# Kernel tuning notes

Hardware: AMD Instinct MI355X
Metric: run time of the kernel (lower is better)

The kernel has to match this reference:

```python
import jax, jax.numpy as jnp
import numpy as np

WH, WW = 7, 7
N = WH * WW
DIM = 384
HEADS = 12
NW = 64          # windows per image
B_ = 2048        # batch * NW


def _relative_position_index():
    ch, cw = np.meshgrid(np.arange(WH), np.arange(WW), indexing='ij')
    coords = np.stack([ch, cw]).reshape(2, -1)                      # [2, N]
    rel = coords[:, :, None] - coords[:, None, :]                   # [2, N, N]
    rel = rel.transpose(1, 2, 0)
    rel[:, :, 0] += WH - 1
    rel[:, :, 1] += WW - 1
    rel[:, :, 0] *= 2 * WW - 1
    return jnp.asarray(rel.sum(-1), dtype=jnp.int32)                # [N, N]


def setup_inputs() -> dict:
    key = jax.random.key(0)
    ks = jax.random.split(key, 7)
    return {
        'x': jax.random.normal(ks[0], (B_, N, DIM), dtype=jnp.float32),
        'qkv_w': jax.random.normal(ks[1], (3 * DIM, DIM), dtype=jnp.float32) * 0.02,
        'qkv_b': jax.random.normal(ks[2], (3 * DIM,), dtype=jnp.float32) * 0.02,
        'proj_w': jax.random.normal(ks[3], (DIM, DIM), dtype=jnp.float32) * 0.02,
        'proj_b': jax.random.normal(ks[4], (DIM,), dtype=jnp.float32) * 0.02,
        'bias_table': jax.random.normal(ks[5], ((2 * WH - 1) * (2 * WW - 1), HEADS), dtype=jnp.float32) * 0.02,
        'mask': jax.random.normal(ks[6], (NW, N, N), dtype=jnp.float32),
        'rel_idx': _relative_position_index(),
    }


def reference(x, qkv_w, qkv_b, proj_w, proj_b, bias_table, mask, rel_idx):
    B_, n, C = x.shape
    H = HEADS
    hd = C // H
    scale = hd ** (-0.5)

    qkv = x @ qkv_w.T + qkv_b                                        # [B_, N, 3C]
    qkv = qkv.reshape(B_, n, 3, H, hd).transpose(2, 0, 3, 1, 4)      # [3, B_, H, N, hd]
    q, k, v = qkv[0], qkv[1], qkv[2]

    attn = jnp.einsum('bhqd,bhkd->bhqk', q * scale, k)               # [B_, H, N, N]

    rpb = bias_table[rel_idx.reshape(-1)].reshape(n, n, H)           # gather [N, N, H]
    attn = attn + rpb.transpose(2, 0, 1)[None]                       # [B_, H, N, N]

    nW = mask.shape[0]
    attn = attn.reshape(B_ // nW, nW, H, n, n) + mask[None, :, None]
    attn = attn.reshape(B_, H, n, n)
    attn = jax.nn.softmax(attn, axis=-1)

    out = jnp.einsum('bhqk,bhkd->bhqd', attn, v)                     # [B_, H, N, hd]
    out = out.transpose(0, 2, 1, 3).reshape(B_, n, C)
    return out @ proj_w.T + proj_b
```

## Files before the change

kernel.cpp:

```cpp
#include <hip/hip_runtime.h>
#include <hip/hip_bf16.h>
#include <cstdint>
#include <cstddef>

#define NTOK 49
#define DIM 384
#define KDIM 384
#define HEADS 12
#define HD 32
#define BATCH 2048
#define MROWS (BATCH * NTOK)

typedef unsigned short u16;
typedef __bf16 bf16x8 __attribute__((ext_vector_type(8)));
typedef unsigned short u16x8 __attribute__((ext_vector_type(8)));
typedef float f32x4 __attribute__((ext_vector_type(4)));

__device__ __forceinline__ u16 f2b(float f) {
  union { float f; unsigned u; } v; v.f = f;
  unsigned r = v.u + 0x7fffu + ((v.u >> 16) & 1u);
  return (u16)(r >> 16);
}

__device__ __forceinline__ bf16x8 ld_bf8(const u16* p) {
  u16x8 u = *(const u16x8*)p;
  return __builtin_bit_cast(bf16x8, u);
}

__device__ __forceinline__ void gload_lds16(const void* g, void* l) {
  __builtin_amdgcn_global_load_lds(
      (const __attribute__((address_space(1))) unsigned*)g,
      (__attribute__((address_space(3))) unsigned*)l, 16, 0, 0);
}

__global__ __launch_bounds__(256) void k_cast(const float* __restrict__ in,
                                              u16* __restrict__ out, int n4) {
  int i = blockIdx.x * 256 + threadIdx.x;
  if (i < n4) {
    float4 v = ((const float4*)in)[i];
    ushort4 o;
    o.x = f2b(v.x); o.y = f2b(v.y); o.z = f2b(v.z); o.w = f2b(v.w);
    ((ushort4*)out)[i] = o;
  }
}

__global__ __launch_bounds__(256) void k_rpbm(const float* __restrict__ bias_table,
                                              const float* __restrict__ mask,
                                              const int* __restrict__ rel_idx,
                                              float* __restrict__ out) {
  int idx = blockIdx.x * 256 + threadIdx.x;
  int r  = idx & 3;
  int l  = (idx >> 2) & 63;
  int ni = (idx >> 8) & 3;
  int mi = (idx >> 10) & 3;
  int w  = (idx >> 12) & 63;
  int h  = idx >> 18;
  int row = mi * 16 + (l >> 4) * 4 + r;
  int col = ni * 16 + (l & 15);
  float v = -1e30f;
  if (row < NTOK && col < NTOK)
    v = bias_table[rel_idx[row * NTOK + col] * HEADS + h] +
        mask[(w * NTOK + row) * NTOK + col];
  out[idx] = v;
}

template <int OUT_BF16, int A_F32, int NCOLS, int NTN, int GD8>
__global__ __launch_bounds__(256) void k_gemm(const void* __restrict__ Av,
                                              const u16* __restrict__ B,
                                              const float* __restrict__ bias,
                                              void* __restrict__ Cv) {
  __shared__ u16 sh[16384];
  int bid = blockIdx.x;
  int tile = (bid & 7) * GD8 + (bid >> 3);
  int mt = tile / NTN, nt = tile - mt * NTN;
  long m0 = (long)mt * 128;
  int n0 = nt * 128;
  int tid = threadIdx.x;
  int lane = tid & 63, wid = tid >> 6;
  int wr = (wid >> 1) * 64, wc = (wid & 1) * 64;
  int c = lane & 15, g = lane >> 4;

  int srow = wid * 16 + (lane >> 2);
  int scol = (lane & 3) * 8;
  const u16* gB = B + (long)(n0 + srow) * KDIM + scol;

  const u16* gA16 = nullptr;
  const float* gAf = nullptr;
  float4 areg[4];
  int arow = tid >> 3;
  int acol = (tid & 7) * 4;
  if (A_F32) {
    gAf = (const float*)Av + (m0 + arow) * KDIM + acol;
#pragma unroll
    for (int rp = 0; rp < 4; ++rp)
      areg[rp] = *(const float4*)(gAf + rp * 32 * KDIM);
  } else {
    gA16 = (const u16*)Av + (m0 + srow) * (long)KDIM + scol;
  }

  f32x4 acc[4][4] = {};

  auto STAGE = [&](int buf, int ktS) {
    u16* As = sh + buf * 8192;
    u16* Bs = As + 4096;
    if (A_F32) {
#pragma unroll
      for (int rp = 0; rp < 4; ++rp) {
        float4 v = areg[rp];
        ushort4 o; o.x = f2b(v.x); o.y = f2b(v.y); o.z = f2b(v.z); o.w = f2b(v.w);
        *(ushort4*)&As[(rp * 32 + arow) * 32 + acol] = o;
      }
      if (ktS + 32 < KDIM) {
#pragma unroll
        for (int rp = 0; rp < 4; ++rp)
          areg[rp] = *(const float4*)(gAf + rp * 32 * KDIM + (ktS + 32));
      }
    } else {
      gload_lds16(gA16 + ktS, &((u16*)As)[srow * 32 + scol]);
      gload_lds16(gA16 + ktS + 64L * KDIM, &((u16*)As)[(srow + 64) * 32 + scol]);
    }
    gload_lds16(gB + ktS, &Bs[srow * 32 + scol]);
    gload_lds16(gB + ktS + 64L * KDIM, &Bs[(srow + 64) * 32 + scol]);
  };

  STAGE(0, 0);
  __syncthreads();
  int cur = 0;
  for (int kt = 0; kt < KDIM; kt += 32) {
    if (kt + 32 < KDIM) STAGE(cur ^ 1, kt + 32);
    const u16* As = sh + cur * 8192;
    const u16* Bs = As + 4096;
    bf16x8 af[4], bfr[4];
#pragma unroll
    for (int i = 0; i < 4; ++i) {
      af[i]  = ld_bf8(&As[(wr + i * 16 + c) * 32 + g * 8]);
      bfr[i] = ld_bf8(&Bs[(wc + i * 16 + c) * 32 + g * 8]);
    }
#pragma unroll
    for (int mi = 0; mi < 4; ++mi)
#pragma unroll
      for (int ni = 0; ni < 4; ++ni)
        acc[mi][ni] = __builtin_amdgcn_mfma_f32_16x16x32_bf16(
            af[mi], bfr[ni], acc[mi][ni], 0, 0, 0);
    __syncthreads();
    cur ^= 1;
  }

  if (OUT_BF16) {
    u16* C = (u16*)Cv;
#pragma unroll
    for (int mi = 0; mi < 4; ++mi)
#pragma unroll
      for (int ni = 0; ni < 4; ++ni) {
        int col = wc + ni * 16 + c;
        float bv = bias[n0 + col];
#pragma unroll
        for (int r = 0; r < 4; ++r) {
          int row = wr + mi * 16 + g * 4 + r;
          sh[row * 128 + col] = f2b(acc[mi][ni][r] + bv);
        }
      }
    __syncthreads();
#pragma unroll
    for (int rep = 0; rep < 8; ++rep) {
      int idx = rep * 2048 + tid * 8;
      int row = idx >> 7, col = idx & 127;
      *(u16x8*)(C + (m0 + row) * NCOLS + n0 + col) = *(const u16x8*)&sh[idx];
    }
  } else {
    float* C = (float*)Cv;
    float* shf = (float*)sh;
#pragma unroll
    for (int chunk = 0; chunk < 2; ++chunk) {
      __syncthreads();
      if ((wr >> 6) == chunk) {
#pragma unroll
        for (int mi = 0; mi < 4; ++mi)
#pragma unroll
          for (int ni = 0; ni < 4; ++ni) {
            int col = wc + ni * 16 + c;
            float bv = bias[n0 + col];
#pragma unroll
            for (int r = 0; r < 4; ++r) {
              int lrow = mi * 16 + g * 4 + r;
              shf[lrow * 128 + col] = acc[mi][ni][r] + bv;
            }
          }
      }
      __syncthreads();
#pragma unroll
      for (int rep = 0; rep < 8; ++rep) {
        int idx = rep * 1024 + tid * 4;
        int row = idx >> 7, col = idx & 127;
        *(float4*)(C + (m0 + chunk * 64 + row) * NCOLS + n0 + col) =
            *(const float4*)&shf[idx];
      }
    }
  }
}

__global__ __launch_bounds__(256) void k_attn(const u16* __restrict__ qkv,
                                              const float* __restrict__ rpbm,
                                              u16* __restrict__ attnout) {
  __shared__ u16 P_lds[4][64 * 64];
  __shared__ u16 vT_lds[4][32 * 64];
  int lane = threadIdx.x & 63, wid = threadIdx.x >> 6;
  int blk = blockIdx.x;
  int w = blk / 96;
  int rr = blk - w * 96;
  int j = rr / 3;
  int hb = rr - j * 3;
  int b = j * 64 + w;
  int h = hb * 4 + wid;
  const u16* base = qkv + (size_t)b * (NTOK * 1152);
  int c = lane & 15, g = lane >> 4;

  u16* vt = vT_lds[wid];
  {
    const u16* vbase = base + 2 * DIM + h * HD;
#pragma unroll
    for (int t = 0; t < 4; ++t) {
      int idx = t * 64 + lane;
      int jj = idx >> 2, d0 = (idx & 3) * 8;
      int jr = jj < NTOK ? jj : NTOK - 1;
      u16x8 vv = *(const u16x8*)(vbase + (size_t)jr * 1152 + d0);
#pragma unroll
      for (int dd = 0; dd < 8; ++dd) {
        int d = d0 + dd;
        int byte = (d * 128 + jj * 2) ^ ((d & 7) << 4);
        *(u16*)((char*)vt + byte) = (u16)vv[dd];
      }
    }
  }

  bf16x8 qa[4], kb[4];
#pragma unroll
  for (int mi = 0; mi < 4; ++mi) {
    int row = mi * 16 + c; if (row > NTOK - 1) row = NTOK - 1;
    qa[mi] = ld_bf8(base + (size_t)row * 1152 + h * HD + g * 8);
  }
#pragma unroll
  for (int ni = 0; ni < 4; ++ni) {
    int row = ni * 16 + c; if (row > NTOK - 1) row = NTOK - 1;
    kb[ni] = ld_bf8(base + (size_t)row * 1152 + DIM + h * HD + g * 8);
  }

  f32x4 s[4][4] = {};
#pragma unroll
  for (int mi = 0; mi < 4; ++mi)
#pragma unroll
    for (int ni = 0; ni < 4; ++ni)
      s[mi][ni] = __builtin_amdgcn_mfma_f32_16x16x32_bf16(qa[mi], kb[ni],
                                                          s[mi][ni], 0, 0, 0);

  const float scale = 0.17677669529663687f;
  const f32x4* rp = (const f32x4*)(rpbm + ((size_t)(h * 64 + w)) * 4096);
#pragma unroll
  for (int mi = 0; mi < 4; ++mi)
#pragma unroll
    for (int ni = 0; ni < 4; ++ni) {
      f32x4 rv = rp[(mi * 4 + ni) * 64 + lane];
#pragma unroll
      for (int r = 0; r < 4; ++r)
        s[mi][ni][r] = s[mi][ni][r] * scale + rv[r];
    }

#pragma unroll
  for (int mi = 0; mi < 4; ++mi)
#pragma unroll
    for (int r = 0; r < 4; ++r) {
      float mx = fmaxf(fmaxf(s[mi][0][r], s[mi][1][r]),
                       fmaxf(s[mi][2][r], s[mi][3][r]));
      mx = fmaxf(mx, __shfl_xor(mx, 1));
      mx = fmaxf(mx, __shfl_xor(mx, 2));
      mx = fmaxf(mx, __shfl_xor(mx, 4));
      mx = fmaxf(mx, __shfl_xor(mx, 8));
      float sum = 0.f;
#pragma unroll
      for (int ni = 0; ni < 4; ++ni) {
        float p = __expf(s[mi][ni][r] - mx);
        s[mi][ni][r] = p;
        sum += p;
      }
      sum += __shfl_xor(sum, 1);
      sum += __shfl_xor(sum, 2);
      sum += __shfl_xor(sum, 4);
      sum += __shfl_xor(sum, 8);
      float inv = __builtin_amdgcn_rcpf(sum);
#pragma unroll
      for (int ni = 0; ni < 4; ++ni) s[mi][ni][r] *= inv;
    }

  u16* pl = P_lds[wid];
#pragma unroll
  for (int mi = 0; mi < 4; ++mi)
#pragma unroll
    for (int ni = 0; ni < 4; ++ni) {
      int col = ni * 16 + c;
#pragma unroll
      for (int r = 0; r < 4; ++r) {
        int row = mi * 16 + g * 4 + r;
        int byte = (row * 128 + col * 2) ^ ((row & 7) << 4);
        *(u16*)((char*)pl + byte) = f2b(s[mi][ni][r]);
      }
    }
  asm volatile("s_waitcnt lgkmcnt(0)" ::: "memory");

  f32x4 o[4][2] = {};
#pragma unroll
  for (int ks = 0; ks < 2; ++ks) {
    bf16x8 vb[2];
#pragma unroll
    for (int n2 = 0; n2 < 2; ++n2) {
      int d = n2 * 16 + c;
      int byte = (d * 128 + ks * 64 + g * 16) ^ ((d & 7) << 4);
      vb[n2] = __builtin_bit_cast(bf16x8, *(const u16x8*)((const char*)vt + byte));
    }
#pragma unroll
    for (int mi = 0; mi < 4; ++mi) {
      int row = mi * 16 + c;
      int byte = (row * 128 + ks * 64 + g * 16) ^ ((row & 7) << 4);
      bf16x8 pa = __builtin_bit_cast(bf16x8, *(const u16x8*)((const char*)pl + byte));
#pragma unroll
      for (int n2 = 0; n2 < 2; ++n2)
        o[mi][n2] = __builtin_amdgcn_mfma_f32_16x16x32_bf16(pa, vb[n2],
                                                            o[mi][n2], 0, 0, 0);
    }
  }

  u16* obase = attnout + (size_t)b * (NTOK * DIM) + h * HD;
#pragma unroll
  for (int mi = 0; mi < 4; ++mi)
#pragma unroll
    for (int r = 0; r < 4; ++r) {
      int row = mi * 16 + g * 4 + r;
      if (row < NTOK) {
#pragma unroll
        for (int n2 = 0; n2 < 2; ++n2)
          obase[(size_t)row * DIM + n2 * 16 + c] = f2b(o[mi][n2][r]);
      }
    }
}

extern "C" void kernel_launch(void* const* d_in, const int* in_sizes, int n_in,
                              void* d_out, int out_size, void* d_ws, size_t ws_size,
                              hipStream_t stream) {
  const float* x       = (const float*)d_in[0];
  const float* qkv_w   = (const float*)d_in[1];
  const float* qkv_b   = (const float*)d_in[2];
  const float* proj_w  = (const float*)d_in[3];
  const float* proj_b  = (const float*)d_in[4];
  const float* bias_tb = (const float*)d_in[5];
  const float* mask    = (const float*)d_in[6];
  const int*   rel_idx = (const int*)d_in[7];
  float* out = (float*)d_out;

  char* ws = (char*)d_ws;
  u16*   wqkvb   = (u16*)(ws + 0);
  u16*   wprojb  = (u16*)(ws + 884736);
  float* rpbm    = (float*)(ws + 1179648);
  u16*   qkv     = (u16*)(ws + 13762560);
  u16*   attnout = (u16*)(ws + 244973568);

  k_cast<<<432, 256, 0, stream>>>(qkv_w, wqkvb, 3 * DIM * DIM / 4);
  k_cast<<<144, 256, 0, stream>>>(proj_w, wprojb, DIM * DIM / 4);

  k_rpbm<<<12288, 256, 0, stream>>>(bias_tb, mask, rel_idx, rpbm);

  k_gemm<1, 1, 1152, 9, 882><<<7056, 256, 0, stream>>>(
      (const void*)x, wqkvb, qkv_b, (void*)qkv);

  k_attn<<<6144, 256, 0, stream>>>(qkv, rpbm, attnout);

  k_gemm<0, 0, 384, 3, 294><<<2352, 256, 0, stream>>>(
      (const void*)attnout, wprojb, proj_b, (void*)out);

  (void)in_sizes; (void)n_in; (void)out_size; (void)ws_size;
}
```

Measured before the change: 377.1 us.

## Pre-cast activations to bf16 in fused prep kernel and use async LDS loads

Merges the weight casts and relative-bias/mask precompute into one prep kernel that also converts the fp32 input activations to bf16 in workspace. The QKV GEMM then loads A with direct global-to-LDS bf16 loads instead of fp32 register loads with in-loop conversion. This removes conversion work and register staging from the GEMM and cuts launch count, but adds a full extra read and write pass over the activation tensor.

Measured after the change: 373.1 us. About the same (-1.1%).

```diff
diff --git a/kernel.cpp b/kernel.cpp
--- a/kernel.cpp
+++ b/kernel.cpp
@@ -33,39 +33,52 @@
       (__attribute__((address_space(3))) unsigned*)l, 16, 0, 0);
 }
 
-__global__ __launch_bounds__(256) void k_cast(const float* __restrict__ in,
-                                              u16* __restrict__ out, int n4) {
-  int i = blockIdx.x * 256 + threadIdx.x;
-  if (i < n4) {
+__global__ __launch_bounds__(256) void k_prep(const float* __restrict__ x,
+                                              u16* __restrict__ xb,
+                                              const float* __restrict__ qkv_w,
+                                              u16* __restrict__ wqkvb,
+                                              const float* __restrict__ proj_w,
+                                              u16* __restrict__ wprojb,
+                                              const float* __restrict__ bias_table,
+                                              const float* __restrict__ mask,
+                                              const int* __restrict__ rel_idx,
+                                              float* __restrict__ rpbm) {
+  int blk = blockIdx.x;
+  if (blk < 38208) {
+    const float* in;
+    u16* out;
+    int i;
+    if (blk < 37632) {
+      in = x; out = xb; i = blk * 256 + threadIdx.x;
+    } else if (blk < 38064) {
+      in = qkv_w; out = wqkvb; i = (blk - 37632) * 256 + threadIdx.x;
+    } else {
+      in = proj_w; out = wprojb; i = (blk - 38064) * 256 + threadIdx.x;
+    }
     float4 v = ((const float4*)in)[i];
     ushort4 o;
     o.x = f2b(v.x); o.y = f2b(v.y); o.z = f2b(v.z); o.w = f2b(v.w);
     ((ushort4*)out)[i] = o;
-  }
-}
-
-__global__ __launch_bounds__(256) void k_rpbm(const float* __restrict__ bias_table,
-                                              const float* __restrict__ mask,
-                                              const int* __restrict__ rel_idx,
-                                              float* __restrict__ out) {
-  int idx = blockIdx.x * 256 + threadIdx.x;
-  int r  = idx & 3;
-  int l  = (idx >> 2) & 63;
-  int ni = (idx >> 8) & 3;
-  int mi = (idx >> 10) & 3;
-  int w  = (idx >> 12) & 63;
-  int h  = idx >> 18;
-  int row = mi * 16 + (l >> 4) * 4 + r;
-  int col = ni * 16 + (l & 15);
-  float v = -1e30f;
-  if (row < NTOK && col < NTOK)
-    v = bias_table[rel_idx[row * NTOK + col] * HEADS + h] +
-        mask[(w * NTOK + row) * NTOK + col];
-  out[idx] = v;
-}
-
-template <int OUT_BF16, int A_F32, int NCOLS, int NTN, int GD8>
-__global__ __launch_bounds__(256) void k_gemm(const void* __restrict__ Av,
+  } else {
+    int idx = (blk - 38208) * 256 + threadIdx.x;
+    int r  = idx & 3;
+    int l  = (idx >> 2) & 63;
+    int ni = (idx >> 8) & 3;
+    int mi = (idx >> 10) & 3;
+    int w  = (idx >> 12) & 63;
+    int h  = idx >> 18;
+    int row = mi * 16 + (l >> 4) * 4 + r;
+    int col = ni * 16 + (l & 15);
+    float v = -1e30f;
+    if (row < NTOK && col < NTOK)
+      v = bias_table[rel_idx[row * NTOK + col] * HEADS + h] +
+          mask[(w * NTOK + row) * NTOK + col];
+    rpbm[idx] = v;
+  }
+}
+
+template <int OUT_BF16, int NCOLS, int NTN, int GD8>
+__global__ __launch_bounds__(256) void k_gemm(const u16* __restrict__ A,
                                               const u16* __restrict__ B,
                                               const float* __restrict__ bias,
                                               void* __restrict__ Cv) {
@@ -82,43 +95,16 @@
 
   int srow = wid * 16 + (lane >> 2);
   int scol = (lane & 3) * 8;
+  const u16* gA = A + (m0 + srow) * (long)KDIM + scol;
   const u16* gB = B + (long)(n0 + srow) * KDIM + scol;
-
-  const u16* gA16 = nullptr;
-  const float* gAf = nullptr;
-  float4 areg[4];
-  int arow = tid >> 3;
-  int acol = (tid & 7) * 4;
-  if (A_F32) {
-    gAf = (const float*)Av + (m0 + arow) * KDIM + acol;
-#pragma unroll
-    for (int rp = 0; rp < 4; ++rp)
-      areg[rp] = *(const float4*)(gAf + rp * 32 * KDIM);
-  } else {
-    gA16 = (const u16*)Av + (m0 + srow) * (long)KDIM + scol;
-  }
 
   f32x4 acc[4][4] = {};
 
   auto STAGE = [&](int buf, int ktS) {
     u16* As = sh + buf * 8192;
     u16* Bs = As + 4096;
-    if (A_F32) {
-#pragma unroll
-      for (int rp = 0; rp < 4; ++rp) {
-        float4 v = areg[rp];
-        ushort4 o; o.x = f2b(v.x); o.y = f2b(v.y); o.z = f2b(v.z); o.w = f2b(v.w);
-        *(ushort4*)&As[(rp * 32 + arow) * 32 + acol] = o;
-      }
-      if (ktS + 32 < KDIM) {
-#pragma unroll
-        for (int rp = 0; rp < 4; ++rp)
-          areg[rp] = *(const float4*)(gAf + rp * 32 * KDIM + (ktS + 32));
-      }
-    } else {
-      gload_lds16(gA16 + ktS, &((u16*)As)[srow * 32 + scol]);
-      gload_lds16(gA16 + ktS + 64L * KDIM, &((u16*)As)[(srow + 64) * 32 + scol]);
-    }
+    gload_lds16(gA + ktS, &As[srow * 32 + scol]);
+    gload_lds16(gA + ktS + 64L * KDIM, &As[(srow + 64) * 32 + scol]);
     gload_lds16(gB + ktS, &Bs[srow * 32 + scol]);
     gload_lds16(gB + ktS + 64L * KDIM, &Bs[(srow + 64) * 32 + scol]);
   };
@@ -356,24 +342,22 @@
   float* out = (float*)d_out;
 
   char* ws = (char*)d_ws;
-  u16*   wqkvb   = (u16*)(ws + 0);
-  u16*   wprojb  = (u16*)(ws + 884736);
-  float* rpbm    = (float*)(ws + 1179648);
-  u16*   qkv     = (u16*)(ws + 13762560);
-  u16*   attnout = (u16*)(ws + 244973568);
-
-  k_cast<<<432, 256, 0, stream>>>(qkv_w, wqkvb, 3 * DIM * DIM / 4);
-  k_cast<<<144, 256, 0, stream>>>(proj_w, wprojb, DIM * DIM / 4);
-
-  k_rpbm<<<12288, 256, 0, stream>>>(bias_tb, mask, rel_idx, rpbm);
-
-  k_gemm<1, 1, 1152, 9, 882><<<7056, 256, 0, stream>>>(
-      (const void*)x, wqkvb, qkv_b, (void*)qkv);
+  u16*   xb      = (u16*)(ws + 0);
+  u16*   wqkvb   = (u16*)(ws + 77070336);
+  u16*   wprojb  = (u16*)(ws + 77955072);
+  float* rpbm    = (float*)(ws + 78249984);
+  u16*   qkv     = (u16*)(ws + 90832896);
+  u16*   attnout = (u16*)(ws + 322043904);
+
+  k_prep<<<50496, 256, 0, stream>>>(x, xb, qkv_w, wqkvb, proj_w, wprojb,
+                                    bias_tb, mask, rel_idx, rpbm);
+
+  k_gemm<1, 1152, 9, 882><<<7056, 256, 0, stream>>>(xb, wqkvb, qkv_b, (void*)qkv);
 
   k_attn<<<6144, 256, 0, stream>>>(qkv, rpbm, attnout);
 
-  k_gemm<0, 0, 384, 3, 294><<<2352, 256, 0, stream>>>(
-      (const void*)attnout, wprojb, proj_b, (void*)out);
+  k_gemm<0, 384, 3, 294><<<2352, 256, 0, stream>>>(attnout, wprojb, proj_b,
+                                                   (void*)out);
 
   (void)in_sizes; (void)n_in; (void)out_size; (void)ws_size;
 }
```
